# Performance work log

Hardware: AMD Instinct MI355X
Metric: run time of the kernel (lower is better)

The kernel has to match this reference:

```python
import jax, jax.numpy as jnp
import numpy as np

B, T, F, D, NL, V = 16, 1024, 80, 512, 3, 28


def _ln(x, g, b, eps=1e-5):
    m = jnp.mean(x, axis=-1, keepdims=True)
    v = jnp.mean((x - m) ** 2, axis=-1, keepdims=True)
    return (x - m) * jax.lax.rsqrt(v + eps) * g + b


def _sru_layer(x, W, wc, bias, g, beta):
    # x: [T, B, din]; W: [din, k*d] (k=4 when din != d, else k=3)
    d = wc.shape[0] // 2
    xn = _ln(x, g, beta)                       # layer_norm=True: LN on layer input
    U = jnp.einsum('tbi,ij->tbj', xn, W)       # [T, B, k*d]
    u0, u1, u2 = U[..., :d], U[..., d:2 * d], U[..., 2 * d:3 * d]
    xres = U[..., 3 * d:4 * d] if W.shape[1] == 4 * d else x  # highway input
    vf, vr = wc[:d], wc[d:]
    bf, br = bias[:d], bias[d:]

    def step(c, inp):
        a0, a1, a2, xr = inp
        f = jax.nn.sigmoid(a1 + vf * c + bf)
        r = jax.nn.sigmoid(a2 + vr * c + br)
        c2 = f * c + (1.0 - f) * a0
        h = r * c2 + (1.0 - r) * xr
        return c2, h

    c0 = jnp.zeros((x.shape[1], d), x.dtype)
    _, h = jax.lax.scan(step, c0, (u0, u1, u2, xres))
    return h


def _lstm_layer(x, wih, whh, bih, bhh):
    # x: [T, B, d]; torch gate order i, f, g, o
    d = whh.shape[1]
    gx = jnp.einsum('tbi,gi->tbg', x, wih) + bih + bhh  # precompute input gates

    def step(carry, gxt):
        h, c = carry
        gts = gxt + h @ whh.T
        i, f, gg, o = jnp.split(gts, 4, axis=-1)
        c2 = jax.nn.sigmoid(f) * c + jax.nn.sigmoid(i) * jnp.tanh(gg)
        h2 = jax.nn.sigmoid(o) * jnp.tanh(c2)
        return (h2, c2), h2

    nb = x.shape[1]
    init = (jnp.zeros((nb, d), x.dtype), jnp.zeros((nb, d), x.dtype))
    _, h = jax.lax.scan(step, init, gx)
    return h


def _forward(x, sru_w0, sru_wc0, sru_b0, sru_ln0_g, sru_ln0_b,
             sru_w, sru_wc, sru_b, sru_ln_g, sru_ln_b,
             lstm_ln_g, lstm_ln_b, lstm_wih, lstm_whh, lstm_bih, lstm_bhh,
             cls_ln_g, cls_ln_b, cls_w):
    h = jnp.transpose(x, (1, 0, 2))  # [T, B, F]
    h = _sru_layer(h, sru_w0, sru_wc0, sru_b0, sru_ln0_g, sru_ln0_b)
    for i in range(sru_w.shape[0]):  # 7 remaining SRU layers (8 total)
        h = _sru_layer(h, sru_w[i], sru_wc[i], sru_b[i], sru_ln_g[i], sru_ln_b[i])
    for i in range(lstm_wih.shape[0]):  # LSTM blocks: LN -> LSTM (dropout off, eval)
        hn = _ln(h, lstm_ln_g[i], lstm_ln_b[i])
        h = _lstm_layer(hn, lstm_wih[i], lstm_whh[i], lstm_bih[i], lstm_bhh[i])
    h = jnp.transpose(h, (1, 0, 2))  # [B, T, D]
    h = _ln(h, cls_ln_g, cls_ln_b)
    return h @ cls_w                 # [B, T, V+1]


def setup_inputs() -> dict:
    key = jax.random.key(0)
    ks = jax.random.split(key, 8)
    n = lambda k, s, sc: jax.random.normal(k, s, jnp.float32) * sc
    sF, sD = 1.0 / np.sqrt(F), 1.0 / np.sqrt(D)
    return {
        'x': n(ks[0], (B, T, F), 1.0),
        'sru_w0': n(ks[1], (F, 4 * D), sF),
        'sru_wc0': n(ks[2], (2 * D,), 0.1),
        'sru_b0': jnp.zeros((2 * D,), jnp.float32),
        'sru_ln0_g': jnp.ones((F,), jnp.float32),
        'sru_ln0_b': jnp.zeros((F,), jnp.float32),
        'sru_w': n(ks[3], (7, D, 3 * D), sD),
        'sru_wc': n(ks[4], (7, 2 * D), 0.1),
        'sru_b': jnp.zeros((7, 2 * D), jnp.float32),
        'sru_ln_g': jnp.ones((7, D), jnp.float32),
        'sru_ln_b': jnp.zeros((7, D), jnp.float32),
        'lstm_ln_g': jnp.ones((NL, D), jnp.float32),
        'lstm_ln_b': jnp.zeros((NL, D), jnp.float32),
        'lstm_wih': n(ks[5], (NL, 4 * D, D), sD),
        'lstm_whh': n(ks[6], (NL, 4 * D, D), sD),
        'lstm_bih': jnp.zeros((NL, 4 * D), jnp.float32),
        'lstm_bhh': jnp.zeros((NL, 4 * D), jnp.float32),
        'cls_ln_g': jnp.ones((D,), jnp.float32),
        'cls_ln_b': jnp.zeros((D,), jnp.float32),
        'cls_w': n(ks[7], (D, V + 1), sD),
    }


def reference(x, sru_w0, sru_wc0, sru_b0, sru_ln0_g, sru_ln0_b,
              sru_w, sru_wc, sru_b, sru_ln_g, sru_ln_b,
              lstm_ln_g, lstm_ln_b, lstm_wih, lstm_whh, lstm_bih, lstm_bhh,
              cls_ln_g, cls_ln_b, cls_w):
    return _forward(x, sru_w0, sru_wc0, sru_b0, sru_ln0_g, sru_ln0_b,
                    sru_w, sru_wc, sru_b, sru_ln_g, sru_ln_b,
                    lstm_ln_g, lstm_ln_b, lstm_wih, lstm_whh, lstm_bih, lstm_bhh,
                    cls_ln_g, cls_ln_b, cls_w)
```

## Files before the change

kernel.cpp:

```cpp
#include <hip/hip_runtime.h>
#include <stdint.h>
#include <stddef.h>

#define B_ 16
#define T_ 1024
#define F_ 80
#define D_ 512
#define M_ 16384
#define VO 29
#define SENT 0x7FC07FC0u
#define GPH 5

typedef float f32x4 __attribute__((ext_vector_type(4)));
typedef short s16x8 __attribute__((ext_vector_type(8)));
typedef unsigned short u16x8 __attribute__((ext_vector_type(8)));

static __device__ __forceinline__ unsigned short f2bf(float f) {
    union { float f; unsigned u; } v; v.f = f;
    unsigned r = v.u + 0x7FFFu + ((v.u >> 16) & 1u);
    return (unsigned short)(r >> 16);
}
static __device__ __forceinline__ float bf2f(unsigned short h) {
    union { unsigned u; float f; } v; v.u = ((unsigned)h) << 16; return v.f;
}
static __device__ __forceinline__ void split2(float v, unsigned short& hi, unsigned short& lo) {
    hi = f2bf(v);
    lo = f2bf(v - bf2f(hi));
}
static __device__ __forceinline__ float sigm(float x) {
    return 1.0f / (1.0f + __expf(-x));
}
static __device__ __forceinline__ float fast_tanh(float x) {
    return 1.0f - 2.0f / (__expf(2.0f * x) + 1.0f);
}
static __device__ __forceinline__ float wred(float v) {
    #pragma unroll
    for (int off = 1; off < 64; off <<= 1) v += __shfl_xor(v, off, 64);
    return v;
}
static __device__ __forceinline__ void stf_agent(float* p, float v) {
    union { float f; unsigned u; } c; c.f = v;
    __hip_atomic_store((unsigned*)p, c.u, __ATOMIC_RELAXED, __HIP_MEMORY_SCOPE_AGENT);
}
static __device__ __forceinline__ void gload16(const void* g, void* lds) {
    __builtin_amdgcn_global_load_lds(
        (const __attribute__((address_space(1))) void*)g,
        (__attribute__((address_space(3))) void*)lds, 16, 0, 0);
}

__global__ __launch_bounds__(256) void conv_w0(const float* __restrict__ W,
        unsigned short* __restrict__ Bh, unsigned short* __restrict__ Bl) {
    int gid = blockIdx.x * 256 + threadIdx.x;
    int n = gid / 96, k = gid - n * 96;
    float v = (k < 80) ? W[(size_t)k * 2048 + n] : 0.0f;
    unsigned short h, l; split2(v, h, l);
    Bh[gid] = h; Bl[gid] = l;
}
__global__ __launch_bounds__(256) void pipe_init(unsigned* __restrict__ rings, int nring,
        unsigned* __restrict__ gxr, int ngx, unsigned* __restrict__ ctl) {
    int total = nring + ngx + 160;
    for (int i = blockIdx.x * 256 + threadIdx.x; i < total; i += gridDim.x * 256) {
        if (i < nring)
            __hip_atomic_store(&rings[i], SENT, __ATOMIC_RELAXED, __HIP_MEMORY_SCOPE_AGENT);
        else if (i < nring + ngx)
            __hip_atomic_store(&gxr[i - nring], SENT, __ATOMIC_RELAXED, __HIP_MEMORY_SCOPE_AGENT);
        else
            __hip_atomic_store(&ctl[i - nring - ngx], 0u, __ATOMIC_RELAXED, __HIP_MEMORY_SCOPE_AGENT);
    }
}

__global__ __launch_bounds__(256) void ln80_kernel(const float* __restrict__ x,
        const float* __restrict__ g, const float* __restrict__ bta,
        unsigned short* __restrict__ xh, unsigned short* __restrict__ xl) {
    int w = threadIdx.x >> 6, lane = threadIdx.x & 63;
    int row = blockIdx.x * 4 + w;
    int b = row & 15, t = row >> 4;
    const float* xr = x + ((size_t)b * T_ + t) * F_;
    float v0 = xr[lane];
    float v1 = (lane < 16) ? xr[64 + lane] : 0.0f;
    float mean = wred(v0 + v1) * (1.0f / 80.0f);
    float d0 = v0 - mean;
    float d1 = (lane < 16) ? (v1 - mean) : 0.0f;
    float var = wred(d0 * d0 + d1 * d1) * (1.0f / 80.0f);
    float rstd = rsqrtf(var + 1e-5f);
    float o0 = d0 * rstd * g[lane] + bta[lane];
    unsigned short h, l; split2(o0, h, l);
    xh[(size_t)row * 96 + lane] = h;
    xl[(size_t)row * 96 + lane] = l;
    if (lane < 32) {
        unsigned short hv = 0, lv = 0;
        if (lane < 16) {
            float o1 = d1 * rstd * g[64 + lane] + bta[64 + lane];
            split2(o1, hv, lv);
        }
        xh[(size_t)row * 96 + 64 + lane] = hv;
        xl[(size_t)row * 96 + 64 + lane] = lv;
    }
}

template <bool LO>
__global__ __launch_bounds__(256) void ln512_bf16(const float* __restrict__ hsrc,
        const float* __restrict__ g, const float* __restrict__ bta,
        unsigned short* __restrict__ oh, unsigned short* __restrict__ ol) {
    int w = threadIdx.x >> 6, lane = threadIdx.x & 63;
    size_t row = (size_t)blockIdx.x * 4 + w;
    const float* hr = hsrc + row * D_;
    float4 p0 = *(const float4*)(hr + lane * 8);
    float4 p1 = *(const float4*)(hr + lane * 8 + 4);
    float s = p0.x + p0.y + p0.z + p0.w + p1.x + p1.y + p1.z + p1.w;
    float mean = wred(s) * (1.0f / 512.0f);
    float d[8] = {p0.x - mean, p0.y - mean, p0.z - mean, p0.w - mean,
                  p1.x - mean, p1.y - mean, p1.z - mean, p1.w - mean};
    float q = 0.f;
    #pragma unroll
    for (int i = 0; i < 8; ++i) q += d[i] * d[i];
    float rstd = rsqrtf(wred(q) * (1.0f / 512.0f) + 1e-5f);
    const float* gp = g + lane * 8;
    const float* bp = bta + lane * 8;
    u16x8 vh, vl;
    #pragma unroll
    for (int i = 0; i < 8; ++i) {
        float o = d[i] * rstd * gp[i] + bp[i];
        unsigned short hh, ll; split2(o, hh, ll);
        vh[i] = hh; vl[i] = ll;
    }
    *(u16x8*)(oh + row * D_ + lane * 8) = vh;
    if (LO) *(u16x8*)(ol + row * D_ + lane * 8) = vl;
}

__global__ __launch_bounds__(256) void ln512_f32(const float* __restrict__ hsrc,
        const float* __restrict__ g, const float* __restrict__ bta,
        float* __restrict__ o) {
    int w = threadIdx.x >> 6, lane = threadIdx.x & 63;
    size_t row = (size_t)blockIdx.x * 4 + w;
    const float* hr = hsrc + row * D_;
    float4 p0 = *(const float4*)(hr + lane * 8);
    float4 p1 = *(const float4*)(hr + lane * 8 + 4);
    float s = p0.x + p0.y + p0.z + p0.w + p1.x + p1.y + p1.z + p1.w;
    float mean = wred(s) * (1.0f / 512.0f);
    float d[8] = {p0.x - mean, p0.y - mean, p0.z - mean, p0.w - mean,
                  p1.x - mean, p1.y - mean, p1.z - mean, p1.w - mean};
    float q = 0.f;
    #pragma unroll
    for (int i = 0; i < 8; ++i) q += d[i] * d[i];
    float rstd = rsqrtf(wred(q) * (1.0f / 512.0f) + 1e-5f);
    const float* gp = g + lane * 8;
    const float* bp = bta + lane * 8;
    float* op = o + row * D_ + lane * 8;
    #pragma unroll
    for (int i = 0; i < 8; ++i) op[i] = d[i] * rstd * gp[i] + bp[i];
}

template <int TERMS>
__global__ __launch_bounds__(256) void gemm_split_t(
        const unsigned short* __restrict__ Ah, const unsigned short* __restrict__ Al,
        const unsigned short* __restrict__ Bh, const unsigned short* __restrict__ Bl,
        float* __restrict__ C, int N, int Kp,
        const float* __restrict__ bias0, const float* __restrict__ bias1) {
    __shared__ __align__(16) unsigned short sAh[4096];
    __shared__ __align__(16) unsigned short sAl[TERMS == 3 ? 4096 : 16];
    __shared__ __align__(16) unsigned short sBh[4096];
    __shared__ __align__(16) unsigned short sBl[4096];
    const int tid = threadIdx.x;
    const int wv = tid >> 6, lane = tid & 63;
    const int c_ = lane & 15, r_ = lane >> 4;
    const int wr = wv >> 1, wc = wv & 1;
    const int mBase = blockIdx.y * 128, nBase = blockIdx.x * 128;

    const int row0 = tid >> 2, row1 = 64 + row0;
    const int sp = tid & 3;
    const int x0 = (row0 & 3) ^ ((row0 >> 2) & 3);
    const int x1 = (row1 & 3) ^ ((row1 >> 2) & 3);
    const size_t gA0 = (size_t)(mBase + row0) * Kp + (size_t)((sp ^ x0) * 8);
    const size_t gA1 = (size_t)(mBase + row1) * Kp + (size_t)((sp ^ x1) * 8);
    const size_t gB0 = (size_t)(nBase + row0) * Kp + (size_t)((sp ^ x0) * 8);
    const size_t gB1 = (size_t)(nBase + row1) * Kp + (size_t)((sp ^ x1) * 8);
    const int ldsW = wv * 1024;

    int offA[4], offB[4];
    #pragma unroll
    for (int f = 0; f < 4; ++f) {
        int ra = wr * 64 + f * 16 + c_;
        int xa = (ra & 3) ^ ((ra >> 2) & 3);
        offA[f] = ra * 32 + ((r_ ^ xa) * 8);
        int rb = wc * 64 + f * 16 + c_;
        int xb = (rb & 3) ^ ((rb >> 2) & 3);
        offB[f] = rb * 32 + ((r_ ^ xb) * 8);
    }

    f32x4 acc[4][4] = {};
    for (int kt = 0; kt < Kp; kt += 32) {
        gload16(Ah + gA0 + kt, (char*)sAh + ldsW);
        gload16(Ah + gA1 + kt, (char*)sAh + 4096 + ldsW);
        if constexpr (TERMS == 3) {
            gload16(Al + gA0 + kt, (char*)sAl + ldsW);
            gload16(Al + gA1 + kt, (char*)sAl + 4096 + ldsW);
        }
        gload16(Bh + gB0 + kt, (char*)sBh + ldsW);
        gload16(Bh + gB1 + kt, (char*)sBh + 4096 + ldsW);
        gload16(Bl + gB0 + kt, (char*)sBl + ldsW);
        gload16(Bl + gB1 + kt, (char*)sBl + 4096 + ldsW);
        __syncthreads();
        s16x8 ah[4], al[4], bh[4], bl[4];
        #pragma unroll
        for (int f = 0; f < 4; ++f) {
            ah[f] = *(const s16x8*)&sAh[offA[f]];
            if constexpr (TERMS == 3) al[f] = *(const s16x8*)&sAl[offA[f]];
            bh[f] = *(const s16x8*)&sBh[offB[f]];
            bl[f] = *(const s16x8*)&sBl[offB[f]];
        }
        #pragma unroll
        for (int mf = 0; mf < 4; ++mf) {
            #pragma unroll
            for (int nf = 0; nf < 4; ++nf) {
                acc[mf][nf] = __builtin_amdgcn_mfma_f32_16x16x32_bf16(ah[mf], bh[nf], acc[mf][nf], 0, 0, 0);
                if constexpr (TERMS == 3)
                    acc[mf][nf] = __builtin_amdgcn_mfma_f32_16x16x32_bf16(al[mf], bh[nf], acc[mf][nf], 0, 0, 0);
                acc[mf][nf] = __builtin_amdgcn_mfma_f32_16x16x32_bf16(ah[mf], bl[nf], acc[mf][nf], 0, 0, 0);
            }
        }
        __syncthreads();
    }
    #pragma unroll
    for (int mf = 0; mf < 4; ++mf) {
        #pragma unroll
        for (int r = 0; r < 4; ++r) {
            int m = mBase + wr * 64 + mf * 16 + r_ * 4 + r;
            float* crow = C + (size_t)m * N + nBase + wc * 64;
            #pragma unroll
            for (int nf = 0; nf < 4; ++nf) {
                int n = nBase + wc * 64 + nf * 16 + c_;
                float v = acc[mf][nf][r];
                if (bias0) v += bias0[n];
                if (bias1) v += bias1[n];
                crow[nf * 16 + c_] = v;
            }
        }
    }
}

__global__ __launch_bounds__(64) void sru_fused(const float* __restrict__ U, int NU,
        const float* __restrict__ xprev, const float* __restrict__ wc,
        const float* __restrict__ bias, float* __restrict__ hout,
        const float* __restrict__ sA, unsigned short* __restrict__ dAh,
        unsigned short* __restrict__ dAl, int nA,
        const float* __restrict__ sB, unsigned short* __restrict__ dBh,
        unsigned short* __restrict__ dBl, int nB,
        const float* __restrict__ sC, unsigned short* __restrict__ dCh,
        unsigned short* __restrict__ dCl, int nC,
        const float* __restrict__ sD, unsigned short* __restrict__ dDh,
        unsigned short* __restrict__ dDl, int nD) {
    const int bid = blockIdx.x;
    if (bid < 128) {
        int gid = bid * 64 + threadIdx.x;
        int d = gid & (D_ - 1), b = gid >> 9;
        float vf = wc[d], vr = wc[D_ + d];
        float bf = bias[d], br = bias[D_ + d];
        const float* u0 = U + d;
        const float* u1 = U + D_ + d;
        const float* u2 = U + 2 * D_ + d;
        const float* xr;  size_t xstride;
        if (xprev) { xr = xprev + d; xstride = D_; }
        else       { xr = U + 3 * (size_t)D_ + d; xstride = (size_t)NU; }
        float* ho = hout + d;
        float c = 0.f;
        #pragma unroll 4
        for (int t = 0; t < T_; ++t) {
            size_t row = (size_t)(t * 16 + b);
            float a0 = u0[row * NU];
            float a1 = u1[row * NU];
            float a2 = u2[row * NU];
            float xv = xr[row * xstride];
            float f = sigm(a1 + vf * c + bf);
            float r = sigm(a2 + vr * c + br);
            c = f * c + (1.f - f) * a0;
            float h = r * c + (1.f - r) * xv;
            ho[row * D_] = h;
        }
    } else {
        const int total = nA + nB + nC + nD;
        const int stride = (2176 - 128) * 64;
        for (int idx = (bid - 128) * 64 + threadIdx.x; idx < total; idx += stride) {
            float v; unsigned short *oh, *ol; int o;
            if (idx < nA) {
                int n = idx >> 9, k = idx & 511;
                v = sA[(size_t)k * 1536 + n]; oh = dAh; ol = dAl; o = idx;
            } else if (idx < nA + nB) {
                o = idx - nA; v = sB[o]; oh = dBh; ol = dBl;
            } else if (idx < nA + nB + nC) {
                o = idx - nA - nB; v = sC[o]; oh = dCh; ol = dCl;
            } else {
                o = idx - nA - nB - nC; v = sD[o]; oh = dDh; ol = dDl;
            }
            unsigned short h, l; split2(v, h, l);
            oh[o] = h; ol[o] = l;
        }
    }
}


template <int MODE>
static __device__ void lstm_role(int wg, const float* gxsrc,
        const unsigned short* Wh, const unsigned short* Wl,
        unsigned* ring, unsigned* myLprog,
        const unsigned* consCprog, float* hout) {
    __shared__ __align__(16) unsigned short hH[16][520];
    __shared__ float G[16][132];
    const int tid = threadIdx.x;
    const int w = tid >> 6, lane = tid & 63;
    const int c_ = lane & 15, r_ = lane >> 4;

    s16x8 bh0[16], bh1[16], bl0[16], bl1[16];
    {
        size_t R0 = (size_t)(w * 512 + wg * 32 + c_) * 512;
        size_t R1 = R0 + 16 * 512;
        #pragma unroll
        for (int ks = 0; ks < 16; ++ks) {
            bh0[ks] = *(const s16x8*)(Wh + R0 + ks * 32 + r_ * 8);
            bh1[ks] = *(const s16x8*)(Wh + R1 + ks * 32 + r_ * 8);
            bl0[ks] = *(const s16x8*)(Wl + R0 + ks * 32 + r_ * 8);
            bl1[ks] = *(const s16x8*)(Wl + R1 + ks * 32 + r_ * 8);
        }
    }
    for (int i = tid; i < 16 * 520; i += 256)
        ((unsigned short*)hH)[i] = 0;
    const int eb = tid >> 4;
    const int ed = (tid * 2) & 31;
    float cc0 = 0.f, cc1 = 0.f;
    const int col0 = w * 512 + wg * 32 + c_;
    const int hidx = (eb * 512 + wg * 32 + ed) >> 1;

    float gxv0[4], gxv1[4];
    if (MODE == 0) {
        #pragma unroll
        for (int r = 0; r < 4; ++r) {
            int bt = r_ * 4 + r;
            gxv0[r] = gxsrc[(size_t)bt * 2048 + col0];
            gxv1[r] = gxsrc[(size_t)bt * 2048 + col0 + 16];
        }
    } else {
        const float* gs = gxsrc;
        unsigned gv[8];
        unsigned gb = 0xFFu;
        while (true) {
            #pragma unroll
            for (int r = 0; r < 4; ++r) {
                int bt = r_ * 4 + r;
                if (gb & (1u << r))
                    gv[r] = __hip_atomic_load((const unsigned*)(gs + (size_t)bt * 2048 + col0),
                                              __ATOMIC_RELAXED, __HIP_MEMORY_SCOPE_AGENT);
                if (gb & (1u << (4 + r)))
                    gv[4 + r] = __hip_atomic_load((const unsigned*)(gs + (size_t)bt * 2048 + col0 + 16),
                                                  __ATOMIC_RELAXED, __HIP_MEMORY_SCOPE_AGENT);
            }
            unsigned nb = 0u;
            #pragma unroll
            for (int r = 0; r < 8; ++r)
                if ((gv[r] >> 16) == 0x7FC0u) nb |= 1u << r;
            gb = nb;
            if (!__any(gb != 0u)) break;
            __builtin_amdgcn_s_sleep(1);
        }
        #pragma unroll
        for (int r = 0; r < 4; ++r) {
            union { unsigned u; float f; } c0, c1;
            c0.u = gv[r]; c1.u = gv[4 + r];
            gxv0[r] = c0.f; gxv1[r] = c1.f;
        }
    }
    int pcur = 0, pnxt = 4096, pthr = 8192;
    __syncthreads();

    for (int t = 0; t < T_; ++t) {
        if (MODE == 1 && tid == 0)
            __hip_atomic_store(&myLprog[wg], (unsigned)t, __ATOMIC_RELAXED, __HIP_MEMORY_SCOPE_AGENT);
        if (consCprog) {
            int lim = t - 1;
            while (true) {
                int p = (int)__hip_atomic_load(&consCprog[lane & 31],
                                               __ATOMIC_RELAXED, __HIP_MEMORY_SCOPE_AGENT);
                if (__all(p >= lim)) break;
                __builtin_amdgcn_s_sleep(2);
            }
        }
        __hip_atomic_store(&ring[pnxt + hidx], SENT, __ATOMIC_RELAXED, __HIP_MEMORY_SCOPE_AGENT);
        f32x4 acc0 = {0.f, 0.f, 0.f, 0.f};
        f32x4 acc1 = {0.f, 0.f, 0.f, 0.f};
        #pragma unroll
        for (int ks = 0; ks < 16; ++ks) {
            s16x8 ah = *(const s16x8*)&hH[c_][ks * 32 + r_ * 8];
            acc0 = __builtin_amdgcn_mfma_f32_16x16x32_bf16(ah, bh0[ks], acc0, 0, 0, 0);
            acc1 = __builtin_amdgcn_mfma_f32_16x16x32_bf16(ah, bh1[ks], acc1, 0, 0, 0);
            acc0 = __builtin_amdgcn_mfma_f32_16x16x32_bf16(ah, bl0[ks], acc0, 0, 0, 0);
            acc1 = __builtin_amdgcn_mfma_f32_16x16x32_bf16(ah, bl1[ks], acc1, 0, 0, 0);
        }
        #pragma unroll
        for (int r = 0; r < 4; ++r) {
            int bt = r_ * 4 + r;
            G[bt][w * 32 + c_]      = acc0[r] + gxv0[r];
            G[bt][w * 32 + 16 + c_] = acc1[r] + gxv1[r];
        }
        __syncthreads();
        float iv0 = G[eb][ed],     fv0 = G[eb][32 + ed], gv0 = G[eb][64 + ed], ov0 = G[eb][96 + ed];
        float iv1 = G[eb][ed + 1], fv1 = G[eb][33 + ed], gv1 = G[eb][65 + ed], ov1 = G[eb][97 + ed];
        cc0 = sigm(fv0) * cc0 + sigm(iv0) * fast_tanh(gv0);
        cc1 = sigm(fv1) * cc1 + sigm(iv1) * fast_tanh(gv1);
        float h0 = sigm(ov0) * fast_tanh(cc0);
        float h1 = sigm(ov1) * fast_tanh(cc1);
        asm volatile("s_waitcnt vmcnt(0)" ::: "memory");
        unsigned packH = (unsigned)f2bf(h0) | ((unsigned)f2bf(h1) << 16);
        __hip_atomic_store(&ring[pcur + hidx], packH, __ATOMIC_RELAXED, __HIP_MEMORY_SCOPE_AGENT);
        if (hout) {
            size_t orow = (size_t)(t * 16 + eb) * D_ + wg * 32 + ed;
            hout[orow] = h0; hout[orow + 1] = h1;
        }
        if (t == T_ - 1) break;
        if (MODE == 0) {
            const float* gxr = gxsrc + (size_t)((t + 1) * 16) * 2048;
            #pragma unroll
            for (int r = 0; r < 4; ++r) {
                int bt = r_ * 4 + r;
                gxv0[r] = gxr[(size_t)bt * 2048 + col0];
                gxv1[r] = gxr[(size_t)bt * 2048 + col0 + 16];
            }
        } else {
            const float* gs = gxsrc + (size_t)((t + 1) % GPH) * 32768;
            unsigned gv[8];
            unsigned gb = 0xFFu;
            while (true) {
                #pragma unroll
                for (int r = 0; r < 4; ++r) {
                    int bt = r_ * 4 + r;
                    if (gb & (1u << r))
                        gv[r] = __hip_atomic_load((const unsigned*)(gs + (size_t)bt * 2048 + col0),
                                                  __ATOMIC_RELAXED, __HIP_MEMORY_SCOPE_AGENT);
                    if (gb & (1u << (4 + r)))
                        gv[4 + r] = __hip_atomic_load((const unsigned*)(gs + (size_t)bt * 2048 + col0 + 16),
                                                      __ATOMIC_RELAXED, __HIP_MEMORY_SCOPE_AGENT);
                }
                unsigned nb = 0u;
                #pragma unroll
                for (int r = 0; r < 8; ++r)
                    if ((gv[r] >> 16) == 0x7FC0u) nb |= 1u << r;
                gb = nb;
                if (!__any(gb != 0u)) break;
                __builtin_amdgcn_s_sleep(1);
            }
            #pragma unroll
            for (int r = 0; r < 4; ++r) {
                union { unsigned u; float f; } c0, c1;
                c0.u = gv[r]; c1.u = gv[4 + r];
                gxv0[r] = c0.f; gxv1[r] = c1.f;
            }
        }
        unsigned long long vh[8];
        unsigned badm = 0xFFu;
        while (true) {
            #pragma unroll
            for (int j = 0; j < 8; ++j) {
                int q = pcur + j * 512 + tid * 2;
                if (badm & (1u << j))
                    vh[j] = __hip_atomic_load((const unsigned long long*)&ring[q],
                                              __ATOMIC_RELAXED, __HIP_MEMORY_SCOPE_AGENT);
            }
            unsigned nb = 0u;
            #pragma unroll
            for (int j = 0; j < 8; ++j) {
                unsigned a0 = (unsigned)vh[j], a1 = (unsigned)(vh[j] >> 32);
                if (((a0 >> 16) == 0x7FC0u) || ((a1 >> 16) == 0x7FC0u)) nb |= 1u << j;
            }
            badm = nb;
            if (!__any(badm != 0u)) break;
            __builtin_amdgcn_s_sleep(1);
        }
        #pragma unroll
        for (int j = 0; j < 8; ++j) {
            int q = j * 512 + tid * 2;
            int bb = q >> 8, dd = (q & 255) * 2;
            *(unsigned long long*)&hH[bb][dd] = vh[j];
        }
        __syncthreads();
        int tmp = pcur; pcur = pnxt; pnxt = pthr; pthr = tmp;
    }
}

static __device__ void crew_role(int cid, const unsigned* srcring, float* gxr,
        unsigned* cprog, const unsigned* lprog,
        const unsigned short* WihHp, const unsigned short* WihLp,
        const float* g, const float* bta,
        const float* bihp, const float* bhhp) {
    __shared__ __align__(16) unsigned short xnH[16][520];
    __shared__ __align__(16) unsigned short xnL[16][520];
    const int tid = threadIdx.x;
    const int w = tid >> 6, lane = tid & 63;
    const int c_ = lane & 15, r_ = lane >> 4;
    const int col = cid * 64 + w * 16 + c_;
    const int rr = w * 4 + r_;

    s16x8 bfh[16], bfl[16];
    {
        const unsigned short* wrH = WihHp + (size_t)col * 512;
        const unsigned short* wrL = WihLp + (size_t)col * 512;
        #pragma unroll
        for (int ks = 0; ks < 16; ++ks) {
            bfh[ks] = *(const s16x8*)(wrH + ks * 32 + r_ * 8);
            bfl[ks] = *(const s16x8*)(wrL + ks * 32 + r_ * 8);
        }
    }
    const float bias = bihp[col] + bhhp[col];
    float lg[32], lb[32];
    #pragma unroll
    for (int j = 0; j < 32; ++j) { lg[j] = g[c_ * 32 + j]; lb[j] = bta[c_ * 32 + j]; }

    for (int t = 0; t < T_; ++t) {
        {
            int lim = t - 3;
            while (true) {
                int p = (int)__hip_atomic_load(&lprog[lane & 15],
                                               __ATOMIC_RELAXED, __HIP_MEMORY_SCOPE_AGENT);
                if (__all(p >= lim)) break;
                __builtin_amdgcn_s_sleep(2);
            }
        }
        {
            unsigned* rs = (unsigned*)(gxr + (size_t)((t + 1) % GPH) * 32768);
            #pragma unroll
            for (int r = 0; r < 4; ++r)
                __hip_atomic_store(&rs[(size_t)(r_ * 4 + r) * 2048 + col], SENT,
                                   __ATOMIC_RELAXED, __HIP_MEMORY_SCOPE_AGENT);
        }
        const unsigned* sb = srcring + (t % 3) * 4096;
        const int qi = rr * 256 + c_ * 16;
        unsigned long long vh[8];
        unsigned badm = 0xFFu;
        while (true) {
            #pragma unroll
            for (int j = 0; j < 8; ++j) {
                if (badm & (1u << j))
                    vh[j] = __hip_atomic_load((const unsigned long long*)&sb[qi + j * 2],
                                              __ATOMIC_RELAXED, __HIP_MEMORY_SCOPE_AGENT);
            }
            unsigned nb = 0u;
            #pragma unroll
            for (int j = 0; j < 8; ++j) {
                unsigned a0 = (unsigned)vh[j], a1 = (unsigned)(vh[j] >> 32);
                if (((a0 >> 16) == 0x7FC0u) || ((a1 >> 16) == 0x7FC0u)) nb |= 1u << j;
            }
            badm = nb;
            if (!__any(badm != 0u)) break;
            __builtin_amdgcn_s_sleep(1);
        }
        float x[32];
        #pragma unroll
        for (int k = 0; k < 8; ++k) {
            unsigned ah = (unsigned)vh[k], bh = (unsigned)(vh[k] >> 32);
            x[4 * k + 0] = bf2f((unsigned short)ah);
            x[4 * k + 1] = bf2f((unsigned short)(ah >> 16));
            x[4 * k + 2] = bf2f((unsigned short)bh);
            x[4 * k + 3] = bf2f((unsigned short)(bh >> 16));
        }
        float s = 0.f;
        #pragma unroll
        for (int j = 0; j < 32; ++j) s += x[j];
        #pragma unroll
        for (int m = 1; m < 16; m <<= 1) s += __shfl_xor(s, m, 64);
        float mean = s * (1.0f / 512.0f);
        float q = 0.f;
        #pragma unroll
        for (int j = 0; j < 32; ++j) { float d = x[j] - mean; q += d * d; }
        #pragma unroll
        for (int m = 1; m < 16; m <<= 1) q += __shfl_xor(q, m, 64);
        float rstd = rsqrtf(q * (1.0f / 512.0f) + 1e-5f);
        u16x8 ph[4], pl[4];
        #pragma unroll
        for (int j = 0; j < 32; ++j) {
            float o = (x[j] - mean) * rstd * lg[j] + lb[j];
            unsigned short hh, ll; split2(o, hh, ll);
            ph[j >> 3][j & 7] = (unsigned short)hh;
            pl[j >> 3][j & 7] = (unsigned short)ll;
        }
        #pragma unroll
        for (int jj = 0; jj < 4; ++jj) {
            *(u16x8*)&xnH[rr][c_ * 32 + jj * 8] = ph[jj];
            *(u16x8*)&xnL[rr][c_ * 32 + jj * 8] = pl[jj];
        }
        __syncthreads();
        if (tid == 0)
            __hip_atomic_store(&cprog[cid], (unsigned)(t + 1), __ATOMIC_RELAXED, __HIP_MEMORY_SCOPE_AGENT);
        f32x4 acc = {bias, bias, bias, bias};
        #pragma unroll
        for (int ks = 0; ks < 16; ++ks) {
            s16x8 axh = *(const s16x8*)&xnH[c_][ks * 32 + r_ * 8];
            s16x8 axl = *(const s16x8*)&xnL[c_][ks * 32 + r_ * 8];
            acc = __builtin_amdgcn_mfma_f32_16x16x32_bf16(axh, bfh[ks], acc, 0, 0, 0);
            acc = __builtin_amdgcn_mfma_f32_16x16x32_bf16(axl, bfh[ks], acc, 0, 0, 0);
            acc = __builtin_amdgcn_mfma_f32_16x16x32_bf16(axh, bfl[ks], acc, 0, 0, 0);
        }
        asm volatile("s_waitcnt vmcnt(0)" ::: "memory");
        float* gs = gxr + (size_t)(t % GPH) * 32768;
        #pragma unroll
        for (int r = 0; r < 4; ++r)
            stf_agent(gs + (size_t)(r_ * 4 + r) * 2048 + col, acc[r]);
        __syncthreads();
    }
}

__global__ __launch_bounds__(256, 1) void lstm_pipe(
        const float* __restrict__ gx0,
        const unsigned short* __restrict__ WhhH, const unsigned short* __restrict__ WhhL,
        const unsigned short* __restrict__ WihH, const unsigned short* __restrict__ WihL,
        const float* __restrict__ lng, const float* __restrict__ lnb,
        const float* __restrict__ bih, const float* __restrict__ bhh,
        float* __restrict__ hout,
        unsigned* __restrict__ rings,
        float* __restrict__ gxr,
        unsigned* __restrict__ ctl) {
    const int bid = blockIdx.x;
    const size_t WSL = (size_t)2048 * 512;
    const int RNG = 3 * 4096;
    if (bid < 16) {
        lstm_role<0>(bid, gx0, WhhH, WhhL, rings,
                     nullptr, ctl + 96, nullptr);
    } else if (bid < 32) {
        lstm_role<1>(bid - 16, gxr, WhhH + WSL, WhhL + WSL, rings + RNG,
                     ctl + 64, ctl + 128, nullptr);
    } else if (bid < 48) {
        lstm_role<1>(bid - 32, gxr + (size_t)GPH * 32768, WhhH + 2 * WSL, WhhL + 2 * WSL,
                     rings + 2 * RNG, ctl + 80, nullptr, hout);
    } else if (bid < 80) {
        crew_role(bid - 48, rings, gxr, ctl + 96, ctl + 64,
                  WihH, WihL, lng + 512, lnb + 512, bih + 2048, bhh + 2048);
    } else {
        crew_role(bid - 80, rings + RNG, gxr + (size_t)GPH * 32768, ctl + 128, ctl + 80,
                  WihH + WSL, WihL + WSL, lng + 1024, lnb + 1024, bih + 4096, bhh + 4096);
    }
}

__global__ __launch_bounds__(256) void cls_gemm(const float* __restrict__ xn,
        const float* __restrict__ wcls, float* __restrict__ out) {
    __shared__ float wl[512][32];
    int tid = threadIdx.x;
    for (int idx = tid; idx < 512 * VO; idx += 256) {
        int k = idx / VO, v = idx - k * VO;
        wl[k][v] = wcls[idx];
    }
    __syncthreads();
    int r8 = tid >> 5, v = tid & 31;
    int row = blockIdx.x * 8 + r8;
    if (v >= VO) return;
    const float* xr = xn + (size_t)row * D_;
    float acc = 0.f;
    #pragma unroll 8
    for (int k = 0; k < 512; ++k) acc += xr[k] * wl[k][v];
    int b = row & 15, t = row >> 4;
    out[((size_t)b * T_ + t) * VO + v] = acc;
}

extern "C" void kernel_launch(void* const* d_in, const int* in_sizes, int n_in,
                              void* d_out, int out_size, void* d_ws, size_t ws_size,
                              hipStream_t stream) {
    const float* x        = (const float*)d_in[0];
    const float* sru_w0   = (const float*)d_in[1];
    const float* sru_wc0  = (const float*)d_in[2];
    const float* sru_b0   = (const float*)d_in[3];
    const float* sru_ln0g = (const float*)d_in[4];
    const float* sru_ln0b = (const float*)d_in[5];
    const float* sru_w    = (const float*)d_in[6];
    const float* sru_wc   = (const float*)d_in[7];
    const float* sru_b    = (const float*)d_in[8];
    const float* sru_lng  = (const float*)d_in[9];
    const float* sru_lnb  = (const float*)d_in[10];
    const float* lstm_lng = (const float*)d_in[11];
    const float* lstm_lnb = (const float*)d_in[12];
    const float* lstm_wih = (const float*)d_in[13];
    const float* lstm_whh = (const float*)d_in[14];
    const float* lstm_bih = (const float*)d_in[15];
    const float* lstm_bhh = (const float*)d_in[16];
    const float* cls_lng  = (const float*)d_in[17];
    const float* cls_lnb  = (const float*)d_in[18];
    const float* cls_w    = (const float*)d_in[19];
    float* out = (float*)d_out;

    char* ws = (char*)d_ws;
    size_t off = 0;
    auto alloc = [&](size_t bytes) -> void* {
        off = (off + 255) & ~(size_t)255;
        void* p = ws + off;
        off += bytes;
        return p;
    };
    float* U             = (float*)alloc((size_t)M_ * 1536 * 4);
    float* hP            = (float*)alloc((size_t)M_ * D_ * 4);
    float* hQ            = (float*)alloc((size_t)M_ * D_ * 4);
    unsigned short* xnh  = (unsigned short*)alloc((size_t)M_ * D_ * 2);
    unsigned short* xnl  = (unsigned short*)alloc((size_t)M_ * D_ * 2);
    unsigned short* w0h  = (unsigned short*)alloc((size_t)2048 * 96 * 2);
    unsigned short* w0l  = (unsigned short*)alloc((size_t)2048 * 96 * 2);
    unsigned short* swh  = (unsigned short*)alloc((size_t)1536 * 512 * 2);
    unsigned short* swl  = (unsigned short*)alloc((size_t)1536 * 512 * 2);
    unsigned short* wihh = (unsigned short*)alloc((size_t)2048 * 512 * 2);
    unsigned short* wihl = (unsigned short*)alloc((size_t)2048 * 512 * 2);
    unsigned short* whh3h = (unsigned short*)alloc((size_t)3 * 2048 * 512 * 2);
    unsigned short* whh3l = (unsigned short*)alloc((size_t)3 * 2048 * 512 * 2);
    unsigned short* wih2h = (unsigned short*)alloc((size_t)2 * 2048 * 512 * 2);
    unsigned short* wih2l = (unsigned short*)alloc((size_t)2 * 2048 * 512 * 2);
    unsigned* rings = (unsigned*)swh;
    float*    gxr   = (float*)swl;
    unsigned* ctl   = (unsigned*)(((char*)swh) + 3 * 3 * 4096 * 4);
    float* gx = U;

    const int WSL = 2048 * 512;
    const int NSW = 1536 * 512;

    hipLaunchKernelGGL(conv_w0, dim3(768), dim3(256), 0, stream, sru_w0, w0h, w0l);

    hipLaunchKernelGGL(ln80_kernel, dim3(4096), dim3(256), 0, stream, x, sru_ln0g, sru_ln0b, xnh, xnl);
    hipLaunchKernelGGL(gemm_split_t<3>, dim3(2048 / 128, M_ / 128), dim3(256), 0, stream,
                       xnh, xnl, w0h, w0l, gx, 2048, 96, (const float*)nullptr, (const float*)nullptr);
    hipLaunchKernelGGL(sru_fused, dim3(2176), dim3(64), 0, stream,
                       gx, 2048, (const float*)nullptr, sru_wc0, sru_b0, hQ,
                       sru_w, swh, swl, NSW,
                       lstm_whh, whh3h, whh3l, 3 * WSL,
                       lstm_wih, wihh, wihl, WSL,
                       lstm_wih + (size_t)WSL, wih2h, wih2l, 2 * WSL);

    float* hcur = hQ; float* hnxt = hP;
    for (int l = 0; l < 7; ++l) {
        hipLaunchKernelGGL(ln512_bf16<false>, dim3(4096), dim3(256), 0, stream,
                           hcur, sru_lng + (size_t)l * 512, sru_lnb + (size_t)l * 512, xnh, xnl);
        hipLaunchKernelGGL(gemm_split_t<2>, dim3(1536 / 128, M_ / 128), dim3(256), 0, stream,
                           xnh, xnh, swh, swl, U, 1536, 512,
                           (const float*)nullptr, (const float*)nullptr);
        int nA = (l < 6) ? NSW : 0;
        hipLaunchKernelGGL(sru_fused, dim3(2176), dim3(64), 0, stream,
                           U, 1536, hcur, sru_wc + (size_t)l * 1024, sru_b + (size_t)l * 1024, hnxt,
                           sru_w + (size_t)(l + 1) * NSW, swh, swl, nA,
                           lstm_whh, whh3h, whh3l, 0,
                           lstm_wih, wihh, wihl, 0,
                           lstm_wih, wih2h, wih2l, 0);
        float* tmp = hcur; hcur = hnxt; hnxt = tmp;
    }

    hipLaunchKernelGGL(ln512_bf16<true>, dim3(4096), dim3(256), 0, stream,
                       hcur, lstm_lng, lstm_lnb, xnh, xnl);
    hipLaunchKernelGGL(gemm_split_t<3>, dim3(2048 / 128, M_ / 128), dim3(256), 0, stream,
                       xnh, xnl, wihh, wihl, gx, 2048, 512, lstm_bih, lstm_bhh);
    hipLaunchKernelGGL(pipe_init, dim3(1024), dim3(256), 0, stream,
                       rings, 3 * 3 * 4096, (unsigned*)gxr, 2 * GPH * 32768, ctl);

    hipLaunchKernelGGL(lstm_pipe, dim3(112), dim3(256), 0, stream,
                       gx, whh3h, whh3l, wih2h, wih2l,
                       lstm_lng, lstm_lnb, lstm_bih, lstm_bhh,
                       hQ, rings, gxr, ctl);

    hipLaunchKernelGGL(ln512_f32, dim3(4096), dim3(256), 0, stream, hQ, cls_lng, cls_lnb, (float*)U);
    hipLaunchKernelGGL(cls_gemm, dim3(2048), dim3(256), 0, stream, (const float*)U, cls_w, out);
}
```

Before: 7.836 ms.

## Fuse SRU projection GEMM with recurrence via per-timeblock completion counters

Each SRU layer's projection GEMM and its sequential recurrence scan now run in one kernel. GEMM blocks publish row tiles with agent-scope stores and bump a per-128-row counter, while 32 scan blocks spin on those counters, so the recurrence starts before the whole GEMM finishes. The weight conversion for the next layer now goes into a double-buffered slot so it can run concurrently, and the pipeline scratch buffers get their own allocations. The cost is spin-waiting, atomic loads, and a dependence on scan blocks being co-resident with GEMM blocks, which risks deadlock or slowdown if scheduling is unfavorable.

```diff
diff --git a/kernel.cpp b/kernel.cpp
--- a/kernel.cpp
+++ b/kernel.cpp
@@ -38,6 +38,10 @@
     for (int off = 1; off < 64; off <<= 1) v += __shfl_xor(v, off, 64);
     return v;
 }
+static __device__ __forceinline__ float ldf_agent(const float* p) {
+    unsigned u = __hip_atomic_load((const unsigned*)p, __ATOMIC_RELAXED, __HIP_MEMORY_SCOPE_AGENT);
+    union { unsigned u; float f; } c; c.u = u; return c.f;
+}
 static __device__ __forceinline__ void stf_agent(float* p, float v) {
     union { float f; unsigned u; } c; c.f = v;
     __hip_atomic_store((unsigned*)p, c.u, __ATOMIC_RELAXED, __HIP_MEMORY_SCOPE_AGENT);
@@ -49,8 +53,11 @@
 }
 
 __global__ __launch_bounds__(256) void conv_w0(const float* __restrict__ W,
-        unsigned short* __restrict__ Bh, unsigned short* __restrict__ Bl) {
+        unsigned short* __restrict__ Bh, unsigned short* __restrict__ Bl,
+        unsigned* __restrict__ cnt) {
     int gid = blockIdx.x * 256 + threadIdx.x;
+    if (gid < 1024)
+        __hip_atomic_store(&cnt[gid], 0u, __ATOMIC_RELAXED, __HIP_MEMORY_SCOPE_AGENT);
     int n = gid / 96, k = gid - n * 96;
     float v = (k < 80) ? W[(size_t)k * 2048 + n] : 0.0f;
     unsigned short h, l; split2(v, h, l);
@@ -239,7 +246,12 @@
     }
 }
 
-__global__ __launch_bounds__(64) void sru_fused(const float* __restrict__ U, int NU,
+template <int TERMS>
+__global__ __launch_bounds__(256) void sru_layer(
+        const unsigned short* __restrict__ Ah, const unsigned short* __restrict__ Al,
+        const unsigned short* __restrict__ Bh, const unsigned short* __restrict__ Bl,
+        float* __restrict__ C, int N, int Kp, int NXT,
+        unsigned* __restrict__ cnt,
         const float* __restrict__ xprev, const float* __restrict__ wc,
         const float* __restrict__ bias, float* __restrict__ hout,
         const float* __restrict__ sA, unsigned short* __restrict__ dAh,
@@ -250,37 +262,122 @@
         unsigned short* __restrict__ dCl, int nC,
         const float* __restrict__ sD, unsigned short* __restrict__ dDh,
         unsigned short* __restrict__ dDl, int nD) {
+    __shared__ __align__(16) unsigned short sAh[4096];
+    __shared__ __align__(16) unsigned short sAl[TERMS == 3 ? 4096 : 16];
+    __shared__ __align__(16) unsigned short sBh[4096];
+    __shared__ __align__(16) unsigned short sBl[4096];
     const int bid = blockIdx.x;
-    if (bid < 128) {
-        int gid = bid * 64 + threadIdx.x;
+    const int tid = threadIdx.x;
+    const int NG = NXT * 128;
+    if (bid < 32) {
+        int gid = bid * 256 + tid;
         int d = gid & (D_ - 1), b = gid >> 9;
         float vf = wc[d], vr = wc[D_ + d];
         float bf = bias[d], br = bias[D_ + d];
-        const float* u0 = U + d;
-        const float* u1 = U + D_ + d;
-        const float* u2 = U + 2 * D_ + d;
-        const float* xr;  size_t xstride;
-        if (xprev) { xr = xprev + d; xstride = D_; }
-        else       { xr = U + 3 * (size_t)D_ + d; xstride = (size_t)NU; }
+        const float* u0 = C + d;
+        const float* u1 = C + D_ + d;
+        const float* u2 = C + 2 * D_ + d;
+        const float* xr;  size_t xstride;  bool xa;
+        if (xprev) { xr = xprev + d; xstride = D_; xa = false; }
+        else       { xr = C + 3 * (size_t)D_ + d; xstride = (size_t)N; xa = true; }
         float* ho = hout + d;
         float c = 0.f;
-        #pragma unroll 4
-        for (int t = 0; t < T_; ++t) {
-            size_t row = (size_t)(t * 16 + b);
-            float a0 = u0[row * NU];
-            float a1 = u1[row * NU];
-            float a2 = u2[row * NU];
-            float xv = xr[row * xstride];
-            float f = sigm(a1 + vf * c + bf);
-            float r = sigm(a2 + vr * c + br);
-            c = f * c + (1.f - f) * a0;
-            float h = r * c + (1.f - r) * xv;
-            ho[row * D_] = h;
-        }
+        for (int tb = 0; tb < 128; ++tb) {
+            while ((int)__hip_atomic_load(&cnt[tb], __ATOMIC_RELAXED, __HIP_MEMORY_SCOPE_AGENT) < NXT)
+                __builtin_amdgcn_s_sleep(2);
+            #pragma unroll
+            for (int j = 0; j < 8; ++j) {
+                int t = tb * 8 + j;
+                size_t row = (size_t)(t * 16 + b);
+                float a0 = ldf_agent(u0 + row * N);
+                float a1 = ldf_agent(u1 + row * N);
+                float a2 = ldf_agent(u2 + row * N);
+                float xv = xa ? ldf_agent(xr + row * xstride) : xr[row * xstride];
+                float f = sigm(a1 + vf * c + bf);
+                float r = sigm(a2 + vr * c + br);
+                c = f * c + (1.f - f) * a0;
+                float h = r * c + (1.f - r) * xv;
+                ho[row * D_] = h;
+            }
+        }
+    } else if (bid < 32 + NG) {
+        const int g = bid - 32;
+        const int nx = g % NXT, my = g / NXT;
+        const int wv = tid >> 6, lane = tid & 63;
+        const int c_ = lane & 15, r_ = lane >> 4;
+        const int wr = wv >> 1, wc_ = wv & 1;
+        const int mBase = my * 128, nBase = nx * 128;
+        const int row0 = tid >> 2, row1 = 64 + row0;
+        const int sp = tid & 3;
+        const int x0 = (row0 & 3) ^ ((row0 >> 2) & 3);
+        const int x1 = (row1 & 3) ^ ((row1 >> 2) & 3);
+        const size_t gA0 = (size_t)(mBase + row0) * Kp + (size_t)((sp ^ x0) * 8);
+        const size_t gA1 = (size_t)(mBase + row1) * Kp + (size_t)((sp ^ x1) * 8);
+        const size_t gB0 = (size_t)(nBase + row0) * Kp + (size_t)((sp ^ x0) * 8);
+        const size_t gB1 = (size_t)(nBase + row1) * Kp + (size_t)((sp ^ x1) * 8);
+        const int ldsW = wv * 1024;
+        int offA[4], offB[4];
+        #pragma unroll
+        for (int f = 0; f < 4; ++f) {
+            int ra = wr * 64 + f * 16 + c_;
+            int xa = (ra & 3) ^ ((ra >> 2) & 3);
+            offA[f] = ra * 32 + ((r_ ^ xa) * 8);
+            int rb = wc_ * 64 + f * 16 + c_;
+            int xb = (rb & 3) ^ ((rb >> 2) & 3);
+            offB[f] = rb * 32 + ((r_ ^ xb) * 8);
+        }
+        f32x4 acc[4][4] = {};
+        for (int kt = 0; kt < Kp; kt += 32) {
+            gload16(Ah + gA0 + kt, (char*)sAh + ldsW);
+            gload16(Ah + gA1 + kt, (char*)sAh + 4096 + ldsW);
+            if constexpr (TERMS == 3) {
+                gload16(Al + gA0 + kt, (char*)sAl + ldsW);
+                gload16(Al + gA1 + kt, (char*)sAl + 4096 + ldsW);
+            }
+            gload16(Bh + gB0 + kt, (char*)sBh + ldsW);
+            gload16(Bh + gB1 + kt, (char*)sBh + 4096 + ldsW);
+            gload16(Bl + gB0 + kt, (char*)sBl + ldsW);
+            gload16(Bl + gB1 + kt, (char*)sBl + 4096 + ldsW);
+            __syncthreads();
+            s16x8 ah[4], al[4], bh[4], bl[4];
+            #pragma unroll
+            for (int f = 0; f < 4; ++f) {
+                ah[f] = *(const s16x8*)&sAh[offA[f]];
+                if constexpr (TERMS == 3) al[f] = *(const s16x8*)&sAl[offA[f]];
+                bh[f] = *(const s16x8*)&sBh[offB[f]];
+                bl[f] = *(const s16x8*)&sBl[offB[f]];
+            }
+            #pragma unroll
+            for (int mf = 0; mf < 4; ++mf) {
+                #pragma unroll
+                for (int nf = 0; nf < 4; ++nf) {
+                    acc[mf][nf] = __builtin_amdgcn_mfma_f32_16x16x32_bf16(ah[mf], bh[nf], acc[mf][nf], 0, 0, 0);
+                    if constexpr (TERMS == 3)
+                        acc[mf][nf] = __builtin_amdgcn_mfma_f32_16x16x32_bf16(al[mf], bh[nf], acc[mf][nf], 0, 0, 0);
+                    acc[mf][nf] = __builtin_amdgcn_mfma_f32_16x16x32_bf16(ah[mf], bl[nf], acc[mf][nf], 0, 0, 0);
+                }
+            }
+            __syncthreads();
+        }
+        #pragma unroll
+        for (int mf = 0; mf < 4; ++mf) {
+            #pragma unroll
+            for (int r = 0; r < 4; ++r) {
+                int m = mBase + wr * 64 + mf * 16 + r_ * 4 + r;
+                float* crow = C + (size_t)m * N + nBase + wc_ * 64;
+                #pragma unroll
+                for (int nf = 0; nf < 4; ++nf)
+                    stf_agent(&crow[nf * 16 + c_], acc[mf][nf][r]);
+            }
+        }
+        asm volatile("s_waitcnt vmcnt(0)" ::: "memory");
+        __syncthreads();
+        if (tid == 0)
+            __hip_atomic_fetch_add(&cnt[my], 1u, __ATOMIC_RELAXED, __HIP_MEMORY_SCOPE_AGENT);
     } else {
         const int total = nA + nB + nC + nD;
-        const int stride = (2176 - 128) * 64;
-        for (int idx = (bid - 128) * 64 + threadIdx.x; idx < total; idx += stride) {
+        const int stride = (gridDim.x - NG - 32) * 256;
+        for (int idx = (bid - NG - 32) * 256 + tid; idx < total; idx += stride) {
             float v; unsigned short *oh, *ol; int o;
             if (idx < nA) {
                 int n = idx >> 9, k = idx & 511;
@@ -696,30 +793,37 @@
     unsigned short* xnl  = (unsigned short*)alloc((size_t)M_ * D_ * 2);
     unsigned short* w0h  = (unsigned short*)alloc((size_t)2048 * 96 * 2);
     unsigned short* w0l  = (unsigned short*)alloc((size_t)2048 * 96 * 2);
-    unsigned short* swh  = (unsigned short*)alloc((size_t)1536 * 512 * 2);
-    unsigned short* swl  = (unsigned short*)alloc((size_t)1536 * 512 * 2);
+    unsigned short* sw0h = (unsigned short*)alloc((size_t)1536 * 512 * 2);
+    unsigned short* sw0l = (unsigned short*)alloc((size_t)1536 * 512 * 2);
+    unsigned short* sw1h = (unsigned short*)alloc((size_t)1536 * 512 * 2);
+    unsigned short* sw1l = (unsigned short*)alloc((size_t)1536 * 512 * 2);
     unsigned short* wihh = (unsigned short*)alloc((size_t)2048 * 512 * 2);
     unsigned short* wihl = (unsigned short*)alloc((size_t)2048 * 512 * 2);
     unsigned short* whh3h = (unsigned short*)alloc((size_t)3 * 2048 * 512 * 2);
     unsigned short* whh3l = (unsigned short*)alloc((size_t)3 * 2048 * 512 * 2);
     unsigned short* wih2h = (unsigned short*)alloc((size_t)2 * 2048 * 512 * 2);
     unsigned short* wih2l = (unsigned short*)alloc((size_t)2 * 2048 * 512 * 2);
-    unsigned* rings = (unsigned*)swh;
-    float*    gxr   = (float*)swl;
-    unsigned* ctl   = (unsigned*)(((char*)swh) + 3 * 3 * 4096 * 4);
+    unsigned* ucnt       = (unsigned*)alloc(1024 * 4);
+    unsigned* rings      = (unsigned*)alloc((size_t)3 * 3 * 4096 * 4);
+    float*    gxr        = (float*)alloc((size_t)2 * GPH * 32768 * 4);
+    unsigned* ctl        = (unsigned*)alloc(256 * 4);
     float* gx = U;
+
+    unsigned short* swh[2] = {sw0h, sw1h};
+    unsigned short* swl[2] = {sw0l, sw1l};
 
     const int WSL = 2048 * 512;
     const int NSW = 1536 * 512;
-
-    hipLaunchKernelGGL(conv_w0, dim3(768), dim3(256), 0, stream, sru_w0, w0h, w0l);
+    const float* nullf = nullptr;
+    unsigned short* nullu = nullptr;
+
+    hipLaunchKernelGGL(conv_w0, dim3(768), dim3(256), 0, stream, sru_w0, w0h, w0l, ucnt);
 
     hipLaunchKernelGGL(ln80_kernel, dim3(4096), dim3(256), 0, stream, x, sru_ln0g, sru_ln0b, xnh, xnl);
-    hipLaunchKernelGGL(gemm_split_t<3>, dim3(2048 / 128, M_ / 128), dim3(256), 0, stream,
-                       xnh, xnl, w0h, w0l, gx, 2048, 96, (const float*)nullptr, (const float*)nullptr);
-    hipLaunchKernelGGL(sru_fused, dim3(2176), dim3(64), 0, stream,
-                       gx, 2048, (const float*)nullptr, sru_wc0, sru_b0, hQ,
-                       sru_w, swh, swl, NSW,
+    hipLaunchKernelGGL(sru_layer<3>, dim3(32 + 16 * 128 + 256), dim3(256), 0, stream,
+                       xnh, xnl, w0h, w0l, gx, 2048, 96, 16, ucnt,
+                       nullf, sru_wc0, sru_b0, hQ,
+                       sru_w, swh[0], swl[0], NSW,
                        lstm_whh, whh3h, whh3l, 3 * WSL,
                        lstm_wih, wihh, wihl, WSL,
                        lstm_wih + (size_t)WSL, wih2h, wih2l, 2 * WSL);
@@ -728,16 +832,15 @@
     for (int l = 0; l < 7; ++l) {
         hipLaunchKernelGGL(ln512_bf16<false>, dim3(4096), dim3(256), 0, stream,
                            hcur, sru_lng + (size_t)l * 512, sru_lnb + (size_t)l * 512, xnh, xnl);
-        hipLaunchKernelGGL(gemm_split_t<2>, dim3(1536 / 128, M_ / 128), dim3(256), 0, stream,
-                           xnh, xnh, swh, swl, U, 1536, 512,
-                           (const float*)nullptr, (const float*)nullptr);
+        int rd = l & 1, wr = (l + 1) & 1;
         int nA = (l < 6) ? NSW : 0;
-        hipLaunchKernelGGL(sru_fused, dim3(2176), dim3(64), 0, stream,
-                           U, 1536, hcur, sru_wc + (size_t)l * 1024, sru_b + (size_t)l * 1024, hnxt,
-                           sru_w + (size_t)(l + 1) * NSW, swh, swl, nA,
-                           lstm_whh, whh3h, whh3l, 0,
-                           lstm_wih, wihh, wihl, 0,
-                           lstm_wih, wih2h, wih2l, 0);
+        hipLaunchKernelGGL(sru_layer<2>, dim3(32 + 12 * 128 + 256), dim3(256), 0, stream,
+                           xnh, xnh, swh[rd], swl[rd], U, 1536, 512, 12, ucnt + 128 * (l + 1),
+                           hcur, sru_wc + (size_t)l * 1024, sru_b + (size_t)l * 1024, hnxt,
+                           sru_w + (size_t)(l + 1) * NSW, swh[wr], swl[wr], nA,
+                           nullf, nullu, nullu, 0,
+                           nullf, nullu, nullu, 0,
+                           nullf, nullu, nullu, 0);
         float* tmp = hcur; hcur = hnxt; hnxt = tmp;
     }
 
```

Result: slower. 8.587 ms (+9.6%).
